# Kernel tuning notes

Hardware: AMD Instinct MI355X
Metric: run time of the kernel (lower is better)

## Reference

```python
import jax, jax.numpy as jnp
import numpy as np

N, E = 50000, 800000
NODE_IN, EDGE_IN, HID, OUT = 64, 16, 64, 32
BN_EPS = 1e-5


def _linear_params(key, fan_in, fan_out):
    kw, kb = jax.random.split(key)
    lim = 1.0 / np.sqrt(fan_in)
    W = jax.random.uniform(kw, (fan_in, fan_out), minval=-lim, maxval=lim, dtype=jnp.float32)
    b = jax.random.uniform(kb, (fan_out,), minval=-lim, maxval=lim, dtype=jnp.float32)
    return W, b


def setup_inputs() -> dict:
    key = jax.random.key(0)
    ks = jax.random.split(key, 8)
    x = jax.random.normal(ks[0], (N, NODE_IN), dtype=jnp.float32)
    edge_index = jax.random.randint(ks[1], (2, E), 0, N, dtype=jnp.int64)
    edge_attr = jax.random.normal(ks[2], (E, EDGE_IN), dtype=jnp.float32)
    # layer 1: message Linear(node_in + edge_in -> hid), self Linear(node_in -> hid)
    W1_msg, b1_msg = _linear_params(ks[3], NODE_IN + EDGE_IN, HID)
    W1_self, b1_self = _linear_params(ks[4], NODE_IN, HID)
    # BatchNorm1d(hidden) params (inference mode: running stats)
    bn_gamma = jnp.ones((HID,), jnp.float32)
    bn_beta = jnp.zeros((HID,), jnp.float32)
    bn_mean = jax.random.normal(ks[5], (HID,), dtype=jnp.float32) * 0.1
    bn_var = jax.random.uniform(ks[6], (HID,), minval=0.5, maxval=1.5, dtype=jnp.float32)
    # layer 2: message Linear(hid + edge_in -> out), self Linear(hid -> out)
    k7, k8 = jax.random.split(ks[7])
    W2_msg, b2_msg = _linear_params(k7, HID + EDGE_IN, OUT)
    W2_self, b2_self = _linear_params(k8, HID, OUT)
    return dict(x=x, edge_index=edge_index, edge_attr=edge_attr,
                W1_msg=W1_msg, b1_msg=b1_msg, W1_self=W1_self, b1_self=b1_self,
                bn_gamma=bn_gamma, bn_beta=bn_beta, bn_mean=bn_mean, bn_var=bn_var,
                W2_msg=W2_msg, b2_msg=b2_msg, W2_self=W2_self, b2_self=b2_self)


def _gnn_layer(x, edge_index, edge_attr, W_msg, b_msg, W_self, b_self):
    # gather source node features per edge, concat edge features, linear, scatter-sum to dst
    src, dst = edge_index[0], edge_index[1]
    m = jnp.concatenate([x[src], edge_attr], axis=-1) @ W_msg + b_msg  # [E, out]
    agg = jax.ops.segment_sum(m, dst, num_segments=x.shape[0])          # [N, out]
    return x @ W_self + b_self + agg


def reference(x, edge_index, edge_attr,
              W1_msg, b1_msg, W1_self, b1_self,
              bn_gamma, bn_beta, bn_mean, bn_var,
              W2_msg, b2_msg, W2_self, b2_self):
    h = _gnn_layer(x, edge_index, edge_attr, W1_msg, b1_msg, W1_self, b1_self)
    # BatchNorm1d (eval mode, running stats) + ReLU; dropout is identity in eval
    h = (h - bn_mean) * jax.lax.rsqrt(bn_var + BN_EPS) * bn_gamma + bn_beta
    h = jax.nn.relu(h)
    return _gnn_layer(h, edge_index, edge_attr, W2_msg, b2_msg, W2_self, b2_self)
```

## Files before the change

kernel.cpp:

```cpp
#include <hip/hip_runtime.h>

#define NN 50000
#define NE 800000
#define NB 6250
#define NT 3125
#define NBK 128
#define BNODE 391
#define BCAP 7680
#define SCAP 56

typedef __attribute__((ext_vector_type(8))) short short8x;
typedef __attribute__((ext_vector_type(4))) float f32x4;

#define OFF_CNT   0LL
#define OFF_ROW   ((long long)NN)
#define OFF_RECS  (3LL*NN + 16)
#define OFF_FLAGS (35LL*NN + 16)
#define OFF_BO    (35LL*NN + 96)
#define OFF_PK    (35LL*NN + 256)
#define OFF_FB1S  (35LL*NN + 7936)
#define OFF_FB2S  (35LL*NN + 8000)
#define OFF_F1    (36LL*NN)
#define OFF_F2    (116LL*NN)
#define OFF_Y2B   (164LL*NN)
#define OFF_S2    (180LL*NN)
#define OFF_BCUR  (212LL*NN)

__device__ __forceinline__ float ldf(const void* p, long long i, int bf16) {
  if (bf16) {
    unsigned short u = ((const unsigned short*)p)[i];
    return __uint_as_float(((unsigned)u) << 16);
  }
  return ((const float*)p)[i];
}
__device__ __forceinline__ unsigned short f2bf(float f) {
  unsigned u = __float_as_uint(f);
  unsigned r = (u + 0x7fffu + ((u >> 16) & 1u)) >> 16;
  return (unsigned short)r;
}
__device__ __forceinline__ unsigned pk2(float lo, float hi) {
  return (unsigned)f2bf(lo) | ((unsigned)f2bf(hi) << 16);
}
__device__ __forceinline__ int ldidx(const void* p, long long i, int i64) {
  return i64 ? (int)((const long long*)p)[i] : ((const int*)p)[i];
}
__device__ __forceinline__ float bflo(unsigned u) { return __uint_as_float(u << 16); }
__device__ __forceinline__ float bfhi(unsigned u) { return __uint_as_float(u & 0xffff0000u); }

__global__ __launch_bounds__(256) void k_prep(
    const void* __restrict__ ei, const void* __restrict__ x,
    const void* __restrict__ W1_msg, const void* __restrict__ b1_msg,
    const void* __restrict__ W1_self, const void* __restrict__ b1_self,
    const void* __restrict__ gamma, const void* __restrict__ beta,
    const void* __restrict__ mean, const void* __restrict__ var,
    const void* __restrict__ W2_msg, const void* __restrict__ b2_msg,
    const void* __restrict__ W2_self, const void* __restrict__ b2_self,
    int* __restrict__ flags, unsigned short* __restrict__ PK,
    float* __restrict__ fb1s, float* __restrict__ fb2s) {
  __shared__ int s_bf;
  int tid = threadIdx.x;
  int lane = tid & 63;
  if (tid < 64) {
    const unsigned short* q = (const unsigned short*)x;
    int cntc = 0;
    for (int i = lane; i < 256; i += 64) {
      unsigned short w = q[2 * i];
      int e = (w >> 7) & 0xff;
      if (w == 0 || (e >= 110 && e <= 140)) cntc++;
    }
    for (int m = 1; m < 64; m <<= 1) cntc += __shfl_xor(cntc, m, 64);
    int bfv = (cntc >= 192) ? 1 : 0;
    if (blockIdx.x == 0) {
      const int* p = (const int*)ei;
      int any = 0;
      for (int i = lane; i < 256; i += 64) any |= p[2 * i + 1];
      unsigned long long anyb = __ballot(any != 0);
      if (lane == 0) {
        flags[0] = (anyb == 0ull) ? 1 : 0;
        flags[1] = bfv;
      }
    }
    if (lane == 0) s_bf = bfv;
  }
  __syncthreads();
  int bf = s_bf;
  int t0 = blockIdx.x * 256 + tid;
  int stride = gridDim.x * 256;
  for (int i = t0; i < 10240; i += stride) {
    int j = i & 7, L = (i >> 3) & 63, t = (i >> 9) & 3, c = i >> 11;
    int k = c * 32 + ((L >> 4) << 3) + j;
    int col = t * 16 + (L & 15);
    float sc = ldf(gamma, col, bf) * rsqrtf(ldf(var, col, bf) + 1e-5f);
    float v;
    if (k < 64) v = ldf(W1_msg, k * 64 + col, bf) * sc;
    else if (k < 128) v = ldf(W1_self, (k - 64) * 64 + col, bf) * sc;
    else if (k < 144) v = ldf(W1_msg, (64 + k - 128) * 64 + col, bf) * sc;
    else if (k == 144) v = ldf(b1_msg, col, bf) * sc;
    else v = 0.0f;
    PK[i] = f2bf(v);
  }
  for (int i = t0; i < 2048; i += stride) {
    int j = i & 7, L = (i >> 3) & 63, t = (i >> 9) & 1, c = i >> 10;
    int k = c * 32 + ((L >> 4) << 3) + j;
    int col = t * 16 + (L & 15);
    PK[10240 + i] = f2bf(ldf(W2_msg, k * 32 + col, bf));
  }
  for (int i = t0; i < 3072; i += stride) {
    int j = i & 7, L = (i >> 3) & 63, t = (i >> 9) & 1, c = i >> 10;
    int k = c * 32 + ((L >> 4) << 3) + j;
    int col = t * 16 + (L & 15);
    float v;
    if (k < 64) v = ldf(W2_self, k * 32 + col, bf);
    else if (k < 80) v = ldf(W2_msg, k * 32 + col, bf);
    else if (k == 80) v = ldf(b2_msg, col, bf);
    else v = 0.0f;
    PK[12288 + i] = f2bf(v);
  }
  for (int i = t0; i < 64; i += stride) {
    float sc = ldf(gamma, i, bf) * rsqrtf(ldf(var, i, bf) + 1e-5f);
    fb1s[i] = ldf(b1_self, i, bf) * sc + ldf(beta, i, bf) - ldf(mean, i, bf) * sc;
  }
  for (int i = t0; i < 32; i += stride) fb2s[i] = ldf(b2_self, i, bf);
}

__global__ __launch_bounds__(256) void k_bin(const void* __restrict__ ei,
                                             const int* __restrict__ flags,
                                             int* __restrict__ bcur,
                                             int2* __restrict__ binbuf) {
  __shared__ int2 stage[NBK][SCAP];
  __shared__ int scnt[NBK];
  __shared__ int gbase[NBK];
  int tid = threadIdx.x;
  for (int i = tid; i < NBK; i += 256) scnt[i] = 0;
  __syncthreads();
  int i64 = flags[0];
  for (long long e0 = (long long)blockIdx.x * 256; e0 < NE;
       e0 += (long long)gridDim.x * 256) {
    long long e = e0 + tid;
    if (e < NE) {
      int src = ldidx(ei, e, i64);
      int dst = ldidx(ei, NE + e, i64);
      int b = dst / BNODE;
      int dl = dst - b * BNODE;
      int2 ent = make_int2(src | (dl << 16), (int)e);
      int pos = atomicAdd(&scnt[b], 1);
      if (pos < SCAP) {
        stage[b][pos] = ent;
      } else {
        int gp = atomicAdd(&bcur[b], 1);
        binbuf[(long long)b * BCAP + gp] = ent;
      }
    }
  }
  __syncthreads();
  if (tid < NBK) {
    int cb = scnt[tid] < SCAP ? scnt[tid] : SCAP;
    gbase[tid] = atomicAdd(&bcur[tid], cb);
  }
  __syncthreads();
  int wv = tid >> 6, ln = tid & 63;
  for (int b = wv; b < NBK; b += 4) {
    int cb = scnt[b] < SCAP ? scnt[b] : SCAP;
    int gb = gbase[b];
    for (int i = ln; i < cb; i += 64)
      binbuf[(long long)b * BCAP + gb + i] = stage[b][i];
  }
}

__global__ __launch_bounds__(1024) void k_place(const int* __restrict__ bcur,
                                                const int2* __restrict__ binbuf,
                                                int* __restrict__ row_ptr,
                                                int2* __restrict__ recs) {
  __shared__ int2 outb[BCAP];
  __shared__ int lh[BNODE];
  __shared__ int lexc[BNODE];
  __shared__ int lcur[BNODE];
  __shared__ int sb[NBK];
  __shared__ int s_rbase;
  int b = blockIdx.x;
  int tid = threadIdx.x;
  int base = b * BNODE;
  int nn = NN - base < BNODE ? NN - base : BNODE;
  if (tid < NBK) sb[tid] = bcur[tid];
  for (int i = tid; i < BNODE; i += 1024) lh[i] = 0;
  __syncthreads();
  if (tid < 64) {
    int v = (tid < b ? sb[tid] : 0) + (tid + 64 < b ? sb[tid + 64] : 0);
    for (int off = 32; off > 0; off >>= 1) v += __shfl_down(v, off, 64);
    if (tid == 0) s_rbase = v;
  }
  int cnt = sb[b];
  __syncthreads();
  int rbase = s_rbase;
  for (int i = tid; i < cnt; i += 1024) {
    int dl = (binbuf[(long long)b * BCAP + i].x >> 16) & 0x3FF;
    atomicAdd(&lh[dl], 1);
  }
  __syncthreads();
  if (tid < 64) {
    int carry = 0;
    for (int c0 = 0; c0 < BNODE; c0 += 64) {
      int i = c0 + tid;
      int orig = (i < nn) ? lh[i] : 0;
      int v = orig;
      for (int off = 1; off < 64; off <<= 1) {
        int u = __shfl_up(v, off, 64);
        if (tid >= off) v += u;
      }
      if (i < nn) lexc[i] = carry + v - orig;
      carry += __shfl(v, 63, 64);
    }
  }
  __syncthreads();
  for (int i = tid; i < nn; i += 1024) {
    int e = lexc[i];
    row_ptr[base + i] = rbase + e;
    lcur[i] = e;
  }
  if (b == NBK - 1 && tid == 0) row_ptr[NN] = rbase + cnt;
  __syncthreads();
  for (int i = tid; i < cnt; i += 1024) {
    int2 ent = binbuf[(long long)b * BCAP + i];
    int dl = (ent.x >> 16) & 0x3FF;
    int p = atomicAdd(&lcur[dl], 1);
    outb[p] = make_int2(ent.x & 0xFFFF, ent.y);
  }
  __syncthreads();
  for (int i = tid; i < cnt; i += 1024) recs[rbase + i] = outb[i];
}

__global__ __launch_bounds__(256) void k_gather1(
    const void* __restrict__ x, const void* __restrict__ ea,
    const int* __restrict__ row_ptr, const int2* __restrict__ recs,
    const int* __restrict__ flags, unsigned short* __restrict__ F1,
    unsigned short* __restrict__ F2) {
  int lane = threadIdx.x & 63;
  int g = lane >> 3, c = lane & 7;
  int bf = flags[1];
  long long wid = ((long long)blockIdx.x * blockDim.x + threadIdx.x) >> 6;
  long long nw = ((long long)gridDim.x * blockDim.x) >> 6;
  for (long long b = wid; b < NB; b += nw) {
    int n = (int)(b * 8 + g);
    int beg = row_ptr[n];
    int deg = row_ptr[n + 1] - beg;
    float a0 = 0.f, a1 = 0.f, a2 = 0.f, a3 = 0.f, a4 = 0.f, a5 = 0.f, a6 = 0.f, a7 = 0.f;
    float e0 = 0.f, e1 = 0.f, e2 = 0.f, e3 = 0.f;
    uint4 xw;
    if (bf) {
      const unsigned short* xs = (const unsigned short*)x;
      const unsigned short* es = (const unsigned short*)ea;
      int t = 0;
      for (; t + 4 <= deg; t += 4) {
        int2 r0 = recs[beg + t + 0];
        int2 r1 = recs[beg + t + 1];
        int2 r2 = recs[beg + t + 2];
        int2 r3 = recs[beg + t + 3];
        uint4 w0 = *((const uint4*)(xs + ((long long)r0.x << 6)) + c);
        uint4 w1 = *((const uint4*)(xs + ((long long)r1.x << 6)) + c);
        uint4 w2 = *((const uint4*)(xs + ((long long)r2.x << 6)) + c);
        uint4 w3 = *((const uint4*)(xs + ((long long)r3.x << 6)) + c);
        a0 += bflo(w0.x) + bflo(w1.x) + bflo(w2.x) + bflo(w3.x);
        a1 += bfhi(w0.x) + bfhi(w1.x) + bfhi(w2.x) + bfhi(w3.x);
        a2 += bflo(w0.y) + bflo(w1.y) + bflo(w2.y) + bflo(w3.y);
        a3 += bfhi(w0.y) + bfhi(w1.y) + bfhi(w2.y) + bfhi(w3.y);
        a4 += bflo(w0.z) + bflo(w1.z) + bflo(w2.z) + bflo(w3.z);
        a5 += bfhi(w0.z) + bfhi(w1.z) + bfhi(w2.z) + bfhi(w3.z);
        a6 += bflo(w0.w) + bflo(w1.w) + bflo(w2.w) + bflo(w3.w);
        a7 += bfhi(w0.w) + bfhi(w1.w) + bfhi(w2.w) + bfhi(w3.w);
        if (c < 4) {
          uint2 q0 = *((const uint2*)(es + ((long long)r0.y << 4)) + c);
          uint2 q1 = *((const uint2*)(es + ((long long)r1.y << 4)) + c);
          uint2 q2 = *((const uint2*)(es + ((long long)r2.y << 4)) + c);
          uint2 q3 = *((const uint2*)(es + ((long long)r3.y << 4)) + c);
          e0 += bflo(q0.x) + bflo(q1.x) + bflo(q2.x) + bflo(q3.x);
          e1 += bfhi(q0.x) + bfhi(q1.x) + bfhi(q2.x) + bfhi(q3.x);
          e2 += bflo(q0.y) + bflo(q1.y) + bflo(q2.y) + bflo(q3.y);
          e3 += bfhi(q0.y) + bfhi(q1.y) + bfhi(q2.y) + bfhi(q3.y);
        }
      }
      for (; t < deg; ++t) {
        int2 r = recs[beg + t];
        uint4 w = *((const uint4*)(xs + ((long long)r.x << 6)) + c);
        a0 += bflo(w.x); a1 += bfhi(w.x);
        a2 += bflo(w.y); a3 += bfhi(w.y);
        a4 += bflo(w.z); a5 += bfhi(w.z);
        a6 += bflo(w.w); a7 += bfhi(w.w);
        if (c < 4) {
          uint2 q = *((const uint2*)(es + ((long long)r.y << 4)) + c);
          e0 += bflo(q.x); e1 += bfhi(q.x);
          e2 += bflo(q.y); e3 += bfhi(q.y);
        }
      }
      xw = *((const uint4*)(xs + ((long long)n << 6)) + c);
    } else {
      const float* xf = (const float*)x;
      const float* ef = (const float*)ea;
      for (int t = 0; t < deg; ++t) {
        int2 r = recs[beg + t];
        float4 w0 = *((const float4*)(xf + ((long long)r.x << 6)) + c * 2);
        float4 w1 = *((const float4*)(xf + ((long long)r.x << 6)) + c * 2 + 1);
        a0 += w0.x; a1 += w0.y; a2 += w0.z; a3 += w0.w;
        a4 += w1.x; a5 += w1.y; a6 += w1.z; a7 += w1.w;
        if (c < 4) {
          float4 q = *((const float4*)(ef + ((long long)r.y << 4)) + c);
          e0 += q.x; e1 += q.y; e2 += q.z; e3 += q.w;
        }
      }
      float4 p0 = *((const float4*)(xf + ((long long)n << 6)) + c * 2);
      float4 p1 = *((const float4*)(xf + ((long long)n << 6)) + c * 2 + 1);
      xw = make_uint4(pk2(p0.x, p0.y), pk2(p0.z, p0.w), pk2(p1.x, p1.y), pk2(p1.z, p1.w));
    }
    unsigned short* f1 = F1 + (long long)n * 160;
    unsigned short* f2 = F2 + (long long)n * 96;
    *((uint4*)f1 + c) = make_uint4(pk2(a0, a1), pk2(a2, a3), pk2(a4, a5), pk2(a6, a7));
    *((uint4*)(f1 + 64) + c) = xw;
    if (c < 4) {
      uint2 sp = make_uint2(pk2(e0, e1), pk2(e2, e3));
      *((uint2*)(f1 + 128) + c) = sp;
      *((uint2*)(f2 + 64) + c) = sp;
    }
    if (c == 4) {
      unsigned d = (unsigned)f2bf((float)deg);
      *((uint4*)(f1 + 144)) = make_uint4(d, 0u, 0u, 0u);
      *((uint4*)(f2 + 80)) = make_uint4(d, 0u, 0u, 0u);
    }
    if (c == 5) {
      *((uint4*)(f1 + 152)) = make_uint4(0u, 0u, 0u, 0u);
      *((uint4*)(f2 + 88)) = make_uint4(0u, 0u, 0u, 0u);
    }
  }
}

__global__ __launch_bounds__(256) void k_gemm1(
    const unsigned short* __restrict__ F1, const unsigned short* __restrict__ PK,
    const float* __restrict__ fb1s, unsigned short* __restrict__ F2,
    unsigned short* __restrict__ Y2B) {
  __shared__ unsigned short hsh[4][16 * 72];
  int lane = threadIdx.x & 63;
  int wv = threadIdx.x >> 6;
  int m = lane & 15, quad = lane >> 4;
  unsigned short* hs = hsh[wv];
  short8x Bf[20];
#pragma unroll
  for (int s = 0; s < 20; ++s) Bf[s] = *(const short8x*)(PK + (s * 64 + lane) * 8);
  short8x By[4];
#pragma unroll
  for (int s = 0; s < 4; ++s) By[s] = *(const short8x*)(PK + 10240 + (s * 64 + lane) * 8);
  long long gw = (long long)blockIdx.x * 4 + wv;
  long long nw = (long long)gridDim.x * 4;
  for (long long tile = gw; tile < NT; tile += nw) {
    long long n0 = tile * 16;
    const unsigned short* f1 = F1 + (n0 + m) * 160 + quad * 8;
    short8x A[5];
#pragma unroll
    for (int cc = 0; cc < 5; ++cc) A[cc] = *(const short8x*)(f1 + cc * 32);
    f32x4 acc[4];
#pragma unroll
    for (int t = 0; t < 4; ++t) {
      float b = fb1s[t * 16 + m];
      acc[t] = (f32x4){b, b, b, b};
    }
#pragma unroll
    for (int cc = 0; cc < 5; ++cc) {
#pragma unroll
      for (int t = 0; t < 4; ++t)
        acc[t] = __builtin_amdgcn_mfma_f32_16x16x32_bf16(A[cc], Bf[cc * 4 + t], acc[t], 0, 0, 0);
    }
#pragma unroll
    for (int t = 0; t < 4; ++t) {
#pragma unroll
      for (int i = 0; i < 4; ++i) {
        float h = fmaxf(acc[t][i], 0.0f);
        unsigned short us = f2bf(h);
        F2[(n0 + quad * 4 + i) * 96 + t * 16 + m] = us;
        hs[(quad * 4 + i) * 72 + t * 16 + m] = us;
      }
    }
    __builtin_amdgcn_sched_barrier(0);
    f32x4 yacc[2];
    yacc[0] = (f32x4){0.f, 0.f, 0.f, 0.f};
    yacc[1] = (f32x4){0.f, 0.f, 0.f, 0.f};
#pragma unroll
    for (int cc = 0; cc < 2; ++cc) {
      short8x Ah = *(const short8x*)(hs + m * 72 + cc * 32 + quad * 8);
#pragma unroll
      for (int t = 0; t < 2; ++t)
        yacc[t] = __builtin_amdgcn_mfma_f32_16x16x32_bf16(Ah, By[cc * 2 + t], yacc[t], 0, 0, 0);
    }
#pragma unroll
    for (int t = 0; t < 2; ++t) {
#pragma unroll
      for (int i = 0; i < 4; ++i)
        Y2B[(n0 + quad * 4 + i) * 32 + t * 16 + m] = f2bf(yacc[t][i]);
    }
    __builtin_amdgcn_sched_barrier(0);
  }
}

__global__ __launch_bounds__(256) void k_gather2(
    const unsigned short* __restrict__ Y2B, const int* __restrict__ row_ptr,
    const int2* __restrict__ recs, float* __restrict__ S2) {
  int lane = threadIdx.x & 63;
  int g = lane >> 3, c = lane & 7;
  long long wid = ((long long)blockIdx.x * blockDim.x + threadIdx.x) >> 6;
  long long nw = ((long long)gridDim.x * blockDim.x) >> 6;
  for (long long b = wid; b < NB; b += nw) {
    int n = (int)(b * 8 + g);
    int beg = row_ptr[n];
    int deg = row_ptr[n + 1] - beg;
    float s0 = 0.f, s1 = 0.f, s2 = 0.f, s3 = 0.f;
    int t = 0;
    for (; t + 4 <= deg; t += 4) {
      int2 r0 = recs[beg + t + 0];
      int2 r1 = recs[beg + t + 1];
      int2 r2 = recs[beg + t + 2];
      int2 r3 = recs[beg + t + 3];
      uint2 q0 = *((const uint2*)(Y2B + (long long)r0.x * 32) + c);
      uint2 q1 = *((const uint2*)(Y2B + (long long)r1.x * 32) + c);
      uint2 q2 = *((const uint2*)(Y2B + (long long)r2.x * 32) + c);
      uint2 q3 = *((const uint2*)(Y2B + (long long)r3.x * 32) + c);
      s0 += bflo(q0.x) + bflo(q1.x) + bflo(q2.x) + bflo(q3.x);
      s1 += bfhi(q0.x) + bfhi(q1.x) + bfhi(q2.x) + bfhi(q3.x);
      s2 += bflo(q0.y) + bflo(q1.y) + bflo(q2.y) + bflo(q3.y);
      s3 += bfhi(q0.y) + bfhi(q1.y) + bfhi(q2.y) + bfhi(q3.y);
    }
    for (; t < deg; ++t) {
      int2 r = recs[beg + t];
      uint2 q = *((const uint2*)(Y2B + (long long)r.x * 32) + c);
      s0 += bflo(q.x); s1 += bfhi(q.x);
      s2 += bflo(q.y); s3 += bfhi(q.y);
    }
    *(float4*)(S2 + (long long)n * 32 + c * 4) = make_float4(s0, s1, s2, s3);
  }
}

__global__ __launch_bounds__(256) void k_gemm2(
    const unsigned short* __restrict__ F2, const unsigned short* __restrict__ PK,
    const float* __restrict__ fb2s, const float* __restrict__ S2,
    const int* __restrict__ flags, void* __restrict__ out) {
  int lane = threadIdx.x & 63;
  int wv = threadIdx.x >> 6;
  int m = lane & 15, quad = lane >> 4;
  int bf = flags[1];
  short8x Bf[6];
#pragma unroll
  for (int s = 0; s < 6; ++s) Bf[s] = *(const short8x*)(PK + 12288 + (s * 64 + lane) * 8);
  long long gw = (long long)blockIdx.x * 4 + wv;
  long long nw = (long long)gridDim.x * 4;
  for (long long tile = gw; tile < NT; tile += nw) {
    long long n0 = tile * 16;
    const unsigned short* f2 = F2 + (n0 + m) * 96 + quad * 8;
    short8x A[3];
#pragma unroll
    for (int cc = 0; cc < 3; ++cc) A[cc] = *(const short8x*)(f2 + cc * 32);
    f32x4 acc[2];
#pragma unroll
    for (int t = 0; t < 2; ++t) {
      float b = fb2s[t * 16 + m];
#pragma unroll
      for (int i = 0; i < 4; ++i)
        acc[t][i] = b + S2[(n0 + quad * 4 + i) * 32 + t * 16 + m];
    }
#pragma unroll
    for (int cc = 0; cc < 3; ++cc) {
#pragma unroll
      for (int t = 0; t < 2; ++t)
        acc[t] = __builtin_amdgcn_mfma_f32_16x16x32_bf16(A[cc], Bf[cc * 2 + t], acc[t], 0, 0, 0);
    }
#pragma unroll
    for (int t = 0; t < 2; ++t) {
#pragma unroll
      for (int i = 0; i < 4; ++i) {
        long long idx = (n0 + quad * 4 + i) * 32 + t * 16 + m;
        if (bf) ((unsigned short*)out)[idx] = f2bf(acc[t][i]);
        else ((float*)out)[idx] = acc[t][i];
      }
    }
  }
}

extern "C" void kernel_launch(void* const* d_in, const int* in_sizes, int n_in,
                              void* d_out, int out_size, void* d_ws, size_t ws_size,
                              hipStream_t stream) {
  const void* x = d_in[0];
  const void* ei = d_in[1];
  const void* ea = d_in[2];
  const void* W1_msg = d_in[3];
  const void* b1_msg = d_in[4];
  const void* W1_self = d_in[5];
  const void* b1_self = d_in[6];
  const void* gamma = d_in[7];
  const void* beta = d_in[8];
  const void* mean = d_in[9];
  const void* var = d_in[10];
  const void* W2_msg = d_in[11];
  const void* b2_msg = d_in[12];
  const void* W2_self = d_in[13];
  const void* b2_self = d_in[14];

  float* ws = (float*)d_ws;
  int* row_ptr = (int*)(ws + OFF_ROW);
  int2* recs = (int2*)(ws + OFF_RECS);
  int* flags = (int*)(ws + OFF_FLAGS);
  unsigned short* PK = (unsigned short*)(ws + OFF_PK);
  float* fb1s = ws + OFF_FB1S;
  float* fb2s = ws + OFF_FB2S;
  unsigned short* F1 = (unsigned short*)(ws + OFF_F1);
  int2* binbuf = (int2*)(ws + OFF_F1);
  unsigned short* F2 = (unsigned short*)(ws + OFF_F2);
  unsigned short* Y2B = (unsigned short*)(ws + OFF_Y2B);
  float* S2 = ws + OFF_S2;
  int* bcur = (int*)(ws + OFF_BCUR);

  hipMemsetAsync(bcur, 0, NBK * sizeof(int), stream);
  hipLaunchKernelGGL(k_prep, dim3(64), dim3(256), 0, stream, ei, x, W1_msg, b1_msg,
                     W1_self, b1_self, gamma, beta, mean, var, W2_msg, b2_msg, W2_self,
                     b2_self, flags, PK, fb1s, fb2s);
  hipLaunchKernelGGL(k_bin, dim3(256), dim3(256), 0, stream, ei, flags, bcur, binbuf);
  hipLaunchKernelGGL(k_place, dim3(NBK), dim3(1024), 0, stream, bcur, binbuf, row_ptr,
                     recs);

  int gblocks = (NB + 3) / 4;
  hipLaunchKernelGGL(k_gather1, dim3(gblocks), dim3(256), 0, stream, x, ea, row_ptr,
                     recs, flags, F1, F2);
  int mblocks = (NT + 3) / 4;
  hipLaunchKernelGGL(k_gemm1, dim3(mblocks), dim3(256), 0, stream, F1, PK, fb1s, F2,
                     Y2B);
  hipLaunchKernelGGL(k_gather2, dim3(gblocks), dim3(256), 0, stream, Y2B, row_ptr, recs,
                     S2);
  hipLaunchKernelGGL(k_gemm2, dim3(mblocks), dim3(256), 0, stream, F2, PK, fb2s, S2,
                     flags, d_out);
}
```

Baseline: 223.5 us.

## Fuse prep with binning and gather2 with gemm2 to cut launches

Merges the weight-packing prep kernel and the edge binning kernel into one launch, with disjoint block ranges doing each job and the bin blocks detecting the index dtype themselves. Also fuses the second-layer neighbour aggregation with the final MFMA GEMM. Aggregated sums now stay in shared memory instead of round-tripping through an S2 buffer in global memory. This removes two kernel launches and one global write/read, at the cost of fixed per-block work splitting (2 tiles per block, half-width MFMA per wave) in the fused second kernel.

```diff
diff --git a/kernel.cpp b/kernel.cpp
--- a/kernel.cpp
+++ b/kernel.cpp
@@ -8,6 +8,8 @@
 #define BNODE 391
 #define BCAP 7680
 #define SCAP 56
+#define BINBLK 256
+#define PREPBLK 64
 
 typedef __attribute__((ext_vector_type(8))) short short8x;
 typedef __attribute__((ext_vector_type(4))) float f32x4;
@@ -16,14 +18,12 @@
 #define OFF_ROW   ((long long)NN)
 #define OFF_RECS  (3LL*NN + 16)
 #define OFF_FLAGS (35LL*NN + 16)
-#define OFF_BO    (35LL*NN + 96)
 #define OFF_PK    (35LL*NN + 256)
 #define OFF_FB1S  (35LL*NN + 7936)
 #define OFF_FB2S  (35LL*NN + 8000)
 #define OFF_F1    (36LL*NN)
 #define OFF_F2    (116LL*NN)
 #define OFF_Y2B   (164LL*NN)
-#define OFF_S2    (180LL*NN)
 #define OFF_BCUR  (212LL*NN)
 
 __device__ __forceinline__ float ldf(const void* p, long long i, int bf16) {
@@ -47,7 +47,7 @@
 __device__ __forceinline__ float bflo(unsigned u) { return __uint_as_float(u << 16); }
 __device__ __forceinline__ float bfhi(unsigned u) { return __uint_as_float(u & 0xffff0000u); }
 
-__global__ __launch_bounds__(256) void k_prep(
+__global__ __launch_bounds__(256) void k_prepbin(
     const void* __restrict__ ei, const void* __restrict__ x,
     const void* __restrict__ W1_msg, const void* __restrict__ b1_msg,
     const void* __restrict__ W1_self, const void* __restrict__ b1_self,
@@ -56,114 +56,119 @@
     const void* __restrict__ W2_msg, const void* __restrict__ b2_msg,
     const void* __restrict__ W2_self, const void* __restrict__ b2_self,
     int* __restrict__ flags, unsigned short* __restrict__ PK,
-    float* __restrict__ fb1s, float* __restrict__ fb2s) {
-  __shared__ int s_bf;
+    float* __restrict__ fb1s, float* __restrict__ fb2s,
+    int* __restrict__ bcur, int2* __restrict__ binbuf) {
   int tid = threadIdx.x;
   int lane = tid & 63;
-  if (tid < 64) {
-    const unsigned short* q = (const unsigned short*)x;
-    int cntc = 0;
-    for (int i = lane; i < 256; i += 64) {
-      unsigned short w = q[2 * i];
-      int e = (w >> 7) & 0xff;
-      if (w == 0 || (e >= 110 && e <= 140)) cntc++;
-    }
-    for (int m = 1; m < 64; m <<= 1) cntc += __shfl_xor(cntc, m, 64);
-    int bfv = (cntc >= 192) ? 1 : 0;
-    if (blockIdx.x == 0) {
+  if (blockIdx.x < BINBLK) {
+    __shared__ int2 stage[NBK][SCAP];
+    __shared__ int scnt[NBK];
+    __shared__ int gbase[NBK];
+    __shared__ int s_i64;
+    for (int i = tid; i < NBK; i += 256) scnt[i] = 0;
+    if (tid < 64) {
       const int* p = (const int*)ei;
       int any = 0;
       for (int i = lane; i < 256; i += 64) any |= p[2 * i + 1];
       unsigned long long anyb = __ballot(any != 0);
-      if (lane == 0) {
-        flags[0] = (anyb == 0ull) ? 1 : 0;
-        flags[1] = bfv;
-      }
-    }
-    if (lane == 0) s_bf = bfv;
-  }
-  __syncthreads();
-  int bf = s_bf;
-  int t0 = blockIdx.x * 256 + tid;
-  int stride = gridDim.x * 256;
-  for (int i = t0; i < 10240; i += stride) {
-    int j = i & 7, L = (i >> 3) & 63, t = (i >> 9) & 3, c = i >> 11;
-    int k = c * 32 + ((L >> 4) << 3) + j;
-    int col = t * 16 + (L & 15);
-    float sc = ldf(gamma, col, bf) * rsqrtf(ldf(var, col, bf) + 1e-5f);
-    float v;
-    if (k < 64) v = ldf(W1_msg, k * 64 + col, bf) * sc;
-    else if (k < 128) v = ldf(W1_self, (k - 64) * 64 + col, bf) * sc;
-    else if (k < 144) v = ldf(W1_msg, (64 + k - 128) * 64 + col, bf) * sc;
-    else if (k == 144) v = ldf(b1_msg, col, bf) * sc;
-    else v = 0.0f;
-    PK[i] = f2bf(v);
-  }
-  for (int i = t0; i < 2048; i += stride) {
-    int j = i & 7, L = (i >> 3) & 63, t = (i >> 9) & 1, c = i >> 10;
-    int k = c * 32 + ((L >> 4) << 3) + j;
-    int col = t * 16 + (L & 15);
-    PK[10240 + i] = f2bf(ldf(W2_msg, k * 32 + col, bf));
-  }
-  for (int i = t0; i < 3072; i += stride) {
-    int j = i & 7, L = (i >> 3) & 63, t = (i >> 9) & 1, c = i >> 10;
-    int k = c * 32 + ((L >> 4) << 3) + j;
-    int col = t * 16 + (L & 15);
-    float v;
-    if (k < 64) v = ldf(W2_self, k * 32 + col, bf);
-    else if (k < 80) v = ldf(W2_msg, k * 32 + col, bf);
-    else if (k == 80) v = ldf(b2_msg, col, bf);
-    else v = 0.0f;
-    PK[12288 + i] = f2bf(v);
-  }
-  for (int i = t0; i < 64; i += stride) {
-    float sc = ldf(gamma, i, bf) * rsqrtf(ldf(var, i, bf) + 1e-5f);
-    fb1s[i] = ldf(b1_self, i, bf) * sc + ldf(beta, i, bf) - ldf(mean, i, bf) * sc;
-  }
-  for (int i = t0; i < 32; i += stride) fb2s[i] = ldf(b2_self, i, bf);
-}
-
-__global__ __launch_bounds__(256) void k_bin(const void* __restrict__ ei,
-                                             const int* __restrict__ flags,
-                                             int* __restrict__ bcur,
-                                             int2* __restrict__ binbuf) {
-  __shared__ int2 stage[NBK][SCAP];
-  __shared__ int scnt[NBK];
-  __shared__ int gbase[NBK];
-  int tid = threadIdx.x;
-  for (int i = tid; i < NBK; i += 256) scnt[i] = 0;
-  __syncthreads();
-  int i64 = flags[0];
-  for (long long e0 = (long long)blockIdx.x * 256; e0 < NE;
-       e0 += (long long)gridDim.x * 256) {
-    long long e = e0 + tid;
-    if (e < NE) {
-      int src = ldidx(ei, e, i64);
-      int dst = ldidx(ei, NE + e, i64);
-      int b = dst / BNODE;
-      int dl = dst - b * BNODE;
-      int2 ent = make_int2(src | (dl << 16), (int)e);
-      int pos = atomicAdd(&scnt[b], 1);
-      if (pos < SCAP) {
-        stage[b][pos] = ent;
-      } else {
-        int gp = atomicAdd(&bcur[b], 1);
-        binbuf[(long long)b * BCAP + gp] = ent;
-      }
-    }
-  }
-  __syncthreads();
-  if (tid < NBK) {
-    int cb = scnt[tid] < SCAP ? scnt[tid] : SCAP;
-    gbase[tid] = atomicAdd(&bcur[tid], cb);
-  }
-  __syncthreads();
-  int wv = tid >> 6, ln = tid & 63;
-  for (int b = wv; b < NBK; b += 4) {
-    int cb = scnt[b] < SCAP ? scnt[b] : SCAP;
-    int gb = gbase[b];
-    for (int i = ln; i < cb; i += 64)
-      binbuf[(long long)b * BCAP + gb + i] = stage[b][i];
+      if (lane == 0) s_i64 = (anyb == 0ull) ? 1 : 0;
+    }
+    __syncthreads();
+    int i64 = s_i64;
+    for (long long e0 = (long long)blockIdx.x * 256; e0 < NE;
+         e0 += (long long)BINBLK * 256) {
+      long long e = e0 + tid;
+      if (e < NE) {
+        int src = ldidx(ei, e, i64);
+        int dst = ldidx(ei, NE + e, i64);
+        int b = dst / BNODE;
+        int dl = dst - b * BNODE;
+        int2 ent = make_int2(src | (dl << 16), (int)e);
+        int pos = atomicAdd(&scnt[b], 1);
+        if (pos < SCAP) {
+          stage[b][pos] = ent;
+        } else {
+          int gp = atomicAdd(&bcur[b], 1);
+          binbuf[(long long)b * BCAP + gp] = ent;
+        }
+      }
+    }
+    __syncthreads();
+    if (tid < NBK) {
+      int cb = scnt[tid] < SCAP ? scnt[tid] : SCAP;
+      gbase[tid] = atomicAdd(&bcur[tid], cb);
+    }
+    __syncthreads();
+    int wv = tid >> 6, ln = tid & 63;
+    for (int b = wv; b < NBK; b += 4) {
+      int cb = scnt[b] < SCAP ? scnt[b] : SCAP;
+      int gb = gbase[b];
+      for (int i = ln; i < cb; i += 64)
+        binbuf[(long long)b * BCAP + gb + i] = stage[b][i];
+    }
+  } else {
+    __shared__ int s_bf;
+    if (tid < 64) {
+      const unsigned short* q = (const unsigned short*)x;
+      int cntc = 0;
+      for (int i = lane; i < 256; i += 64) {
+        unsigned short w = q[2 * i];
+        int e = (w >> 7) & 0xff;
+        if (w == 0 || (e >= 110 && e <= 140)) cntc++;
+      }
+      for (int m = 1; m < 64; m <<= 1) cntc += __shfl_xor(cntc, m, 64);
+      int bfv = (cntc >= 192) ? 1 : 0;
+      if (blockIdx.x == BINBLK) {
+        const int* p = (const int*)ei;
+        int any = 0;
+        for (int i = lane; i < 256; i += 64) any |= p[2 * i + 1];
+        unsigned long long anyb = __ballot(any != 0);
+        if (lane == 0) {
+          flags[0] = (anyb == 0ull) ? 1 : 0;
+          flags[1] = bfv;
+        }
+      }
+      if (lane == 0) s_bf = bfv;
+    }
+    __syncthreads();
+    int bf = s_bf;
+    int t0 = (blockIdx.x - BINBLK) * 256 + tid;
+    int stride = PREPBLK * 256;
+    for (int i = t0; i < 10240; i += stride) {
+      int j = i & 7, L = (i >> 3) & 63, t = (i >> 9) & 3, c = i >> 11;
+      int k = c * 32 + ((L >> 4) << 3) + j;
+      int col = t * 16 + (L & 15);
+      float sc = ldf(gamma, col, bf) * rsqrtf(ldf(var, col, bf) + 1e-5f);
+      float v;
+      if (k < 64) v = ldf(W1_msg, k * 64 + col, bf) * sc;
+      else if (k < 128) v = ldf(W1_self, (k - 64) * 64 + col, bf) * sc;
+      else if (k < 144) v = ldf(W1_msg, (64 + k - 128) * 64 + col, bf) * sc;
+      else if (k == 144) v = ldf(b1_msg, col, bf) * sc;
+      else v = 0.0f;
+      PK[i] = f2bf(v);
+    }
+    for (int i = t0; i < 2048; i += stride) {
+      int j = i & 7, L = (i >> 3) & 63, t = (i >> 9) & 1, c = i >> 10;
+      int k = c * 32 + ((L >> 4) << 3) + j;
+      int col = t * 16 + (L & 15);
+      PK[10240 + i] = f2bf(ldf(W2_msg, k * 32 + col, bf));
+    }
+    for (int i = t0; i < 3072; i += stride) {
+      int j = i & 7, L = (i >> 3) & 63, t = (i >> 9) & 1, c = i >> 10;
+      int k = c * 32 + ((L >> 4) << 3) + j;
+      int col = t * 16 + (L & 15);
+      float v;
+      if (k < 64) v = ldf(W2_self, k * 32 + col, bf);
+      else if (k < 80) v = ldf(W2_msg, k * 32 + col, bf);
+      else if (k == 80) v = ldf(b2_msg, col, bf);
+      else v = 0.0f;
+      PK[12288 + i] = f2bf(v);
+    }
+    for (int i = t0; i < 64; i += stride) {
+      float sc = ldf(gamma, i, bf) * rsqrtf(ldf(var, i, bf) + 1e-5f);
+      fb1s[i] = ldf(b1_self, i, bf) * sc + ldf(beta, i, bf) - ldf(mean, i, bf) * sc;
+    }
+    for (int i = t0; i < 32; i += stride) fb2s[i] = ldf(b2_self, i, bf);
   }
 }
 
@@ -397,15 +402,22 @@
   }
 }
 
-__global__ __launch_bounds__(256) void k_gather2(
-    const unsigned short* __restrict__ Y2B, const int* __restrict__ row_ptr,
-    const int2* __restrict__ recs, float* __restrict__ S2) {
-  int lane = threadIdx.x & 63;
-  int g = lane >> 3, c = lane & 7;
-  long long wid = ((long long)blockIdx.x * blockDim.x + threadIdx.x) >> 6;
-  long long nw = ((long long)gridDim.x * blockDim.x) >> 6;
-  for (long long b = wid; b < NB; b += nw) {
-    int n = (int)(b * 8 + g);
+__global__ __launch_bounds__(256) void k_gg2(
+    const unsigned short* __restrict__ F2, const unsigned short* __restrict__ PK,
+    const float* __restrict__ fb2s, const unsigned short* __restrict__ Y2B,
+    const int* __restrict__ row_ptr, const int2* __restrict__ recs,
+    const int* __restrict__ flags, void* __restrict__ out) {
+  __shared__ float sums[2][16][33];
+  int tid = threadIdx.x;
+  int lane = tid & 63;
+  int wv = tid >> 6;
+  int tp = wv >> 1;
+  int th = wv & 1;
+  long long tile = (long long)blockIdx.x * 2 + tp;
+  int valid = tile < NT;
+  if (valid) {
+    int g = lane >> 3, c = lane & 7;
+    int n = (int)(tile * 16 + th * 8 + g);
     int beg = row_ptr[n];
     int deg = row_ptr[n + 1] - beg;
     float s0 = 0.f, s1 = 0.f, s2 = 0.f, s3 = 0.f;
@@ -430,51 +442,34 @@
       s0 += bflo(q.x); s1 += bfhi(q.x);
       s2 += bflo(q.y); s3 += bfhi(q.y);
     }
-    *(float4*)(S2 + (long long)n * 32 + c * 4) = make_float4(s0, s1, s2, s3);
-  }
-}
-
-__global__ __launch_bounds__(256) void k_gemm2(
-    const unsigned short* __restrict__ F2, const unsigned short* __restrict__ PK,
-    const float* __restrict__ fb2s, const float* __restrict__ S2,
-    const int* __restrict__ flags, void* __restrict__ out) {
-  int lane = threadIdx.x & 63;
-  int wv = threadIdx.x >> 6;
-  int m = lane & 15, quad = lane >> 4;
-  int bf = flags[1];
-  short8x Bf[6];
-#pragma unroll
-  for (int s = 0; s < 6; ++s) Bf[s] = *(const short8x*)(PK + 12288 + (s * 64 + lane) * 8);
-  long long gw = (long long)blockIdx.x * 4 + wv;
-  long long nw = (long long)gridDim.x * 4;
-  for (long long tile = gw; tile < NT; tile += nw) {
+    float* sr = &sums[tp][th * 8 + g][c * 4];
+    sr[0] = s0; sr[1] = s1; sr[2] = s2; sr[3] = s3;
+  }
+  __syncthreads();
+  if (valid) {
+    int m = lane & 15, quad = lane >> 4;
+    int bf = flags[1];
     long long n0 = tile * 16;
     const unsigned short* f2 = F2 + (n0 + m) * 96 + quad * 8;
     short8x A[3];
 #pragma unroll
     for (int cc = 0; cc < 3; ++cc) A[cc] = *(const short8x*)(f2 + cc * 32);
-    f32x4 acc[2];
-#pragma unroll
-    for (int t = 0; t < 2; ++t) {
-      float b = fb2s[t * 16 + m];
-#pragma unroll
-      for (int i = 0; i < 4; ++i)
-        acc[t][i] = b + S2[(n0 + quad * 4 + i) * 32 + t * 16 + m];
-    }
-#pragma unroll
-    for (int cc = 0; cc < 3; ++cc) {
-#pragma unroll
-      for (int t = 0; t < 2; ++t)
-        acc[t] = __builtin_amdgcn_mfma_f32_16x16x32_bf16(A[cc], Bf[cc * 2 + t], acc[t], 0, 0, 0);
-    }
-#pragma unroll
-    for (int t = 0; t < 2; ++t) {
-#pragma unroll
-      for (int i = 0; i < 4; ++i) {
-        long long idx = (n0 + quad * 4 + i) * 32 + t * 16 + m;
-        if (bf) ((unsigned short*)out)[idx] = f2bf(acc[t][i]);
-        else ((float*)out)[idx] = acc[t][i];
-      }
+    short8x Bf[3];
+#pragma unroll
+    for (int cc = 0; cc < 3; ++cc)
+      Bf[cc] = *(const short8x*)(PK + 12288 + ((cc * 2 + th) * 64 + lane) * 8);
+    f32x4 acc;
+    float fb = fb2s[th * 16 + m];
+#pragma unroll
+    for (int i = 0; i < 4; ++i) acc[i] = fb + sums[tp][quad * 4 + i][th * 16 + m];
+#pragma unroll
+    for (int cc = 0; cc < 3; ++cc)
+      acc = __builtin_amdgcn_mfma_f32_16x16x32_bf16(A[cc], Bf[cc], acc, 0, 0, 0);
+#pragma unroll
+    for (int i = 0; i < 4; ++i) {
+      long long idx = (n0 + quad * 4 + i) * 32 + th * 16 + m;
+      if (bf) ((unsigned short*)out)[idx] = f2bf(acc[i]);
+      else ((float*)out)[idx] = acc[i];
     }
   }
 }
@@ -509,14 +504,12 @@
   int2* binbuf = (int2*)(ws + OFF_F1);
   unsigned short* F2 = (unsigned short*)(ws + OFF_F2);
   unsigned short* Y2B = (unsigned short*)(ws + OFF_Y2B);
-  float* S2 = ws + OFF_S2;
   int* bcur = (int*)(ws + OFF_BCUR);
 
   hipMemsetAsync(bcur, 0, NBK * sizeof(int), stream);
-  hipLaunchKernelGGL(k_prep, dim3(64), dim3(256), 0, stream, ei, x, W1_msg, b1_msg,
-                     W1_self, b1_self, gamma, beta, mean, var, W2_msg, b2_msg, W2_self,
-                     b2_self, flags, PK, fb1s, fb2s);
-  hipLaunchKernelGGL(k_bin, dim3(256), dim3(256), 0, stream, ei, flags, bcur, binbuf);
+  hipLaunchKernelGGL(k_prepbin, dim3(BINBLK + PREPBLK), dim3(256), 0, stream, ei, x,
+                     W1_msg, b1_msg, W1_self, b1_self, gamma, beta, mean, var, W2_msg,
+                     b2_msg, W2_self, b2_self, flags, PK, fb1s, fb2s, bcur, binbuf);
   hipLaunchKernelGGL(k_place, dim3(NBK), dim3(1024), 0, stream, bcur, binbuf, row_ptr,
                      recs);
 
@@ -526,8 +519,6 @@
   int mblocks = (NT + 3) / 4;
   hipLaunchKernelGGL(k_gemm1, dim3(mblocks), dim3(256), 0, stream, F1, PK, fb1s, F2,
                      Y2B);
-  hipLaunchKernelGGL(k_gather2, dim3(gblocks), dim3(256), 0, stream, Y2B, row_ptr, recs,
-                     S2);
-  hipLaunchKernelGGL(k_gemm2, dim3(mblocks), dim3(256), 0, stream, F2, PK, fb2s, S2,
-                     flags, d_out);
-}
+  hipLaunchKernelGGL(k_gg2, dim3((NT + 1) / 2), dim3(256), 0, stream, F2, PK, fb2s,
+                     Y2B, row_ptr, recs, flags, d_out);
+}
```

After: 212.3 us. -5.0%, faster.
